# Optimization experiments

Measured on AMD Instinct MI355X. Metric: run time of the kernel, lower is better.

The kernel has to match this reference:

```python
import jax, jax.numpy as jnp
import numpy as np

B, S, D = 1, 2048, 2048
N_HEAD, N_KV = 32, 8
HD = D // N_HEAD  # 64


def make_freqs_cis(seq_len, head_dim, base=10000.0):
    inv = 1.0 / (base ** (np.arange(0, head_dim, 2, dtype=np.float32) / head_dim))
    t = np.arange(seq_len, dtype=np.float32)
    f = np.outer(t, inv)  # [S, HD/2]
    return jnp.asarray(np.stack([np.cos(f), np.sin(f)], axis=-1))  # [S, HD/2, 2]


def setup_inputs() -> dict:
    key = jax.random.key(0)
    k1, k2, k3 = jax.random.split(key, 3)
    scale = 1.0 / np.sqrt(D)
    return {
        "hidden_states": jax.random.normal(k1, (B, S, D), jnp.float32),
        "freqs_cis": make_freqs_cis(S, HD),
        "wqkv": jax.random.normal(k2, ((N_HEAD + 2 * N_KV) * HD, D), jnp.float32) * scale,
        "wo": jax.random.normal(k3, (D, D), jnp.float32) * scale,
    }


def apply_rotary(x, freqs_cis):
    # x: [B, S, H, HD]; freqs_cis: [S, HD/2, 2]
    xs = x.reshape(*x.shape[:-1], HD // 2, 2)
    cos = freqs_cis[None, :, None, :, 0]
    sin = freqs_cis[None, :, None, :, 1]
    x0, x1 = xs[..., 0], xs[..., 1]
    out = jnp.stack([x0 * cos - x1 * sin, x1 * cos + x0 * sin], axis=-1)
    return out.reshape(x.shape)


def reference(hidden_states, freqs_cis, wqkv, wo):
    bsz, seq_len, _ = hidden_states.shape
    kv_size = N_KV * HD
    qkv = hidden_states @ wqkv.T  # [B, S, 3072]
    q, k, v = jnp.split(qkv, [D, D + kv_size], axis=-1)
    q = q.reshape(bsz, seq_len, N_HEAD, HD)
    k = k.reshape(bsz, seq_len, N_KV, HD)
    v = v.reshape(bsz, seq_len, N_KV, HD)
    q = apply_rotary(q, freqs_cis)
    k = apply_rotary(k, freqs_cis)
    # [B, H, S, HD]
    q = q.transpose(0, 2, 1, 3)
    k = k.transpose(0, 2, 1, 3)
    v = v.transpose(0, 2, 1, 3)
    rep = N_HEAD // N_KV
    k = jnp.repeat(k, rep, axis=1)
    v = jnp.repeat(v, rep, axis=1)
    scores = jnp.einsum("bhqd,bhkd->bhqk", q, k) / jnp.sqrt(jnp.float32(HD))
    causal = jnp.tril(jnp.ones((seq_len, seq_len), bool))
    scores = jnp.where(causal[None, None], scores, jnp.finfo(scores.dtype).min)
    attn = jax.nn.softmax(scores, axis=-1)
    out = jnp.einsum("bhqk,bhkd->bhqd", attn, v)
    out = out.transpose(0, 2, 1, 3).reshape(bsz, seq_len, D)
    return out @ wo.T
```

## Files before the change

kernel.cpp:

```cpp
#include <hip/hip_runtime.h>

typedef unsigned short u16;
typedef __attribute__((ext_vector_type(8))) short bf16x8;
typedef __attribute__((ext_vector_type(4))) float f32x4;

#define MFMA16(a, b, c) __builtin_amdgcn_mfma_f32_16x16x32_bf16((a), (b), (c), 0, 0, 0)
#define EXP2(x) __builtin_amdgcn_exp2f(x)

#define S 2048
#define D 2048
#define NH 32
#define NKV 8
#define HD 64
#define QKV_N 3072

__device__ __forceinline__ u16 f2bf(float f) {
  unsigned int u = __float_as_uint(f);
  u += 0x7fffu + ((u >> 16) & 1u);
  return (u16)(u >> 16);
}

__device__ __forceinline__ void glds16(const void* g, void* l) {
  __builtin_amdgcn_global_load_lds((const __attribute__((address_space(1))) unsigned int*)g,
                                   (__attribute__((address_space(3))) unsigned int*)l,
                                   16, 0, 0);
}

__device__ __forceinline__ unsigned int cvtpk(float lo, float hi) {
  unsigned int r;
  asm("v_cvt_pk_bf16_f32 %0, %1, %2" : "=v"(r) : "v"(lo), "v"(hi));
  return r;
}
__device__ __forceinline__ void swap32(unsigned int& a, unsigned int& b) {
  asm("v_permlane32_swap_b32 %0, %1" : "+v"(a), "+v"(b));
}
__device__ __forceinline__ void swap16(unsigned int& a, unsigned int& b) {
  asm("v_permlane16_swap_b32 %0, %1" : "+v"(a), "+v"(b));
}
__device__ __forceinline__ bf16x8 pack4(const f32x4 c0, const f32x4 c1) {
  unsigned int x0 = cvtpk(c0[0], c0[1]);
  unsigned int x1 = cvtpk(c0[2], c0[3]);
  unsigned int y0 = cvtpk(c1[0], c1[1]);
  unsigned int y1 = cvtpk(c1[2], c1[3]);
  swap32(x0, y0); swap16(x0, y0);
  swap32(x1, y1); swap16(x1, y1);
  union { bf16x8 v; unsigned int u[4]; } r;
  r.u[0] = x0; r.u[1] = x1; r.u[2] = y0; r.u[3] = y1;
  return r.v;
}

#define N1 (S * D / 4)
#define N2 (QKV_N * D / 4)
#define N3 (D * D / 4)
__global__ void cast_all(const float* __restrict__ hs, const float* __restrict__ wqkv,
                         const float* __restrict__ wo, u16* __restrict__ o1,
                         u16* __restrict__ o2, u16* __restrict__ o3) {
  int i = blockIdx.x * blockDim.x + threadIdx.x;
  const float* src;
  u16* dst;
  int idx;
  if (i < N1) { src = hs; dst = o1; idx = i; }
  else if (i < N1 + N2) { src = wqkv; dst = o2; idx = i - N1; }
  else if (i < N1 + N2 + N3) { src = wo; dst = o3; idx = i - N1 - N2; }
  else return;
  float4 v = ((const float4*)src)[idx];
  ushort4 o;
  o.x = f2bf(v.x); o.y = f2bf(v.y); o.z = f2bf(v.z); o.w = f2bf(v.w);
  ((ushort4*)dst)[idx] = o;
}

#define GEMM_MAINLOOP(A_, B_, K_, bm_, bn_)                                            \
  const int srowS = lane >> 3, scolS = ((lane & 7) ^ srowS) * 8;                       \
  const int aBase = wave * 32, bBase = wave * 16;                                      \
  const int qq = lane >> 4, sw = lr & 7;                                               \
  _Pragma("unroll") for (int c2 = 0; c2 < 4; ++c2)                                     \
      glds16(A_ + (size_t)(bm_ + aBase + c2 * 8 + srowS) * K_ + scolS,                 \
             &sA[0][aBase + c2 * 8][0]);                                               \
  _Pragma("unroll") for (int c2 = 0; c2 < 2; ++c2)                                     \
      glds16(B_ + (size_t)(bn_ + bBase + c2 * 8 + srowS) * K_ + scolS,                 \
             &sB[0][bBase + c2 * 8][0]);                                               \
  const int nk = K_ >> 6;                                                              \
  for (int it = 0; it < nk; ++it) {                                                    \
    const int buf = it & 1;                                                            \
    __syncthreads();                                                                   \
    if (it + 1 < nk) {                                                                 \
      const int k1 = (it + 1) << 6;                                                    \
      _Pragma("unroll") for (int c2 = 0; c2 < 4; ++c2)                                 \
          glds16(A_ + (size_t)(bm_ + aBase + c2 * 8 + srowS) * K_ + k1 + scolS,        \
                 &sA[buf ^ 1][aBase + c2 * 8][0]);                                     \
      _Pragma("unroll") for (int c2 = 0; c2 < 2; ++c2)                                 \
          glds16(B_ + (size_t)(bn_ + bBase + c2 * 8 + srowS) * K_ + k1 + scolS,        \
                 &sB[buf ^ 1][bBase + c2 * 8][0]);                                     \
    }                                                                                  \
    bf16x8 af[2][2], bfr[2][4];                                                        \
    _Pragma("unroll") for (int c = 0; c < 2; ++c) {                                    \
      const int pc = (((c << 2) | qq) ^ sw) * 8;     \
      _Pragma("unroll") for (int i = 0; i < 2; ++i)                                    \
          af[c][i] = *(const bf16x8*)(&sA[buf][wr + i * 16 + lr][pc]);                 \
      _Pragma("unroll") for (int j = 0; j < 4; ++j)                                    \
          bfr[c][j] = *(const bf16x8*)(&sB[buf][j * 16 + lr][pc]);                     \
    }                                                                                  \
    _Pragma("unroll") for (int c = 0; c < 2; ++c)                                      \
        _Pragma("unroll") for (int i = 0; i < 2; ++i)                                  \
            _Pragma("unroll") for (int j = 0; j < 4; ++j)                              \
                acc[i][j] = MFMA16(af[c][i], bfr[c][j], acc[i][j]);                    \
  }

__global__ __launch_bounds__(256) void gemm_bt(const u16* __restrict__ A, const u16* __restrict__ B,
                                               float* __restrict__ C, int M, int N, int K) {
  __shared__ u16 sA[2][128][64];
  __shared__ u16 sB[2][64][64];
  const int tid = threadIdx.x;
  const int wave = tid >> 6, lane = tid & 63;
  const int bm = blockIdx.y * 128, bn = blockIdx.x * 64;
  const int lr = lane & 15, lk = (lane >> 4) * 8;
  const int wr = wave * 32;
  (void)lk;

  f32x4 acc[2][4] = {};
  GEMM_MAINLOOP(A, B, K, bm, bn)

  const int crb = (lane >> 4) * 4;
#pragma unroll
  for (int i = 0; i < 2; ++i)
#pragma unroll
    for (int j = 0; j < 4; ++j)
#pragma unroll
      for (int r = 0; r < 4; ++r) {
        int row = bm + wr + i * 16 + crb + r;
        int col = bn + j * 16 + lr;
        C[(size_t)row * N + col] = acc[i][j][r];
      }
}

#define QSCALE 0.18033688011112042f
__global__ __launch_bounds__(256) void gemm1_fused(const u16* __restrict__ A, const u16* __restrict__ B,
                                                   const float* __restrict__ fc,
                                                   u16* __restrict__ qo, u16* __restrict__ ko,
                                                   u16* __restrict__ vt) {
  __shared__ u16 sA[2][128][64];
  __shared__ u16 sB[2][64][64];
  const int tid = threadIdx.x;
  const int wave = tid >> 6, lane = tid & 63;
  const int bm = blockIdx.y * 128, bn = blockIdx.x * 64;
  const int lr = lane & 15, lk = (lane >> 4) * 8;
  const int wr = wave * 32;
  (void)lk;

  f32x4 acc[2][4] = {};
  GEMM_MAINLOOP(A, B, D, bm, bn)

  const int crb = (lane >> 4) * 4;

  if (bn < 2560) {
    const bool isQ = (bn < 2048);
    u16* dst_base = isQ ? (qo + (size_t)(bn >> 6) * S * HD)
                        : (ko + (size_t)((bn - 2048) >> 6) * S * HD);
    const float scale = isQ ? QSCALE : 1.0f;
    const int odd = lr & 1;
#pragma unroll
    for (int i = 0; i < 2; ++i)
#pragma unroll
      for (int r = 0; r < 4; ++r) {
        const int srow = bm + wr + i * 16 + crb + r;
#pragma unroll
        for (int j = 0; j < 4; ++j) {
          const int d = j * 16 + lr;
          float x = acc[i][j][r];
          float xp = __shfl_xor(x, 1, 64);
          float2 cs = *(const float2*)(fc + (size_t)srow * 64 + (d >> 1) * 2);
          float y = odd ? (x * cs.x + xp * cs.y) : (x * cs.x - xp * cs.y);
          dst_base[(size_t)srow * HD + d] = f2bf(y * scale);
        }
      }
  } else {
    const int kvh = (bn - 2560) >> 6;
    __syncthreads();
    u16(*sT)[136] = (u16(*)[136]) & sA[0][0][0];
#pragma unroll
    for (int i = 0; i < 2; ++i)
#pragma unroll
      for (int j = 0; j < 4; ++j)
#pragma unroll
        for (int r = 0; r < 4; ++r)
          sT[j * 16 + lr][wr + i * 16 + crb + r] = f2bf(acc[i][j][r]);
    __syncthreads();
    const int d = tid >> 2, sc = (tid & 3) * 32;
    uint4* dst = (uint4*)(vt + (size_t)kvh * HD * S + (size_t)d * S + bm + sc);
    const uint4* src = (const uint4*)(&sT[d][sc]);
    dst[0] = src[0];
    dst[1] = src[1];
    dst[2] = src[2];
    dst[3] = src[3];
  }
}

__global__ __launch_bounds__(256, 2) void attn_kernel(const u16* __restrict__ Q, const u16* __restrict__ Kc,
                                                      const u16* __restrict__ Vt, u16* __restrict__ Out) {
  __shared__ u16 sK[2][64][64];
  __shared__ u16 sV[2][64][64];

  const int h = blockIdx.y;
  const int p = (h >= 16) ? (15 - blockIdx.x) : blockIdx.x;
  const int kvh = h >> 2;
  const int tid = threadIdx.x;
  const int wave = tid >> 6, lane = tid & 63;
  const int lr = lane & 15;
  const int hi = lane >> 4;
  const int lk = hi * 8;
  const int crb = hi * 4;
  const int sw = lr & 7;
  const int pcK0 = (hi ^ sw) * 8;
  const int pcK1 = ((4 | hi) ^ sw) * 8;
  const int t = 4 * p + wave;
  const int qbA = 16 * t;
  const int qbB = 16 * (127 - t);

  const u16* qpA = Q + ((size_t)h * S + qbA + lr) * HD;
  const u16* qpB = Q + ((size_t)h * S + qbB + lr) * HD;
  bf16x8 aA0 = *(const bf16x8*)(qpA + lk);
  bf16x8 aA1 = *(const bf16x8*)(qpA + 32 + lk);
  bf16x8 aB0 = *(const bf16x8*)(qpB + lk);
  bf16x8 aB1 = *(const bf16x8*)(qpB + 32 + lk);

  const u16* Kh = Kc + (size_t)kvh * S * HD;
  const u16* Vh = Vt + (size_t)kvh * HD * S;

  const int sr0 = tid >> 3, so0 = (tid & 7) * 8;
  const int sr1 = sr0 + 32;
  const int swz = (((tid & 7) ^ (sr0 & 7)) << 3);

  f32x4 lAv = {}, lBv = {};
  f32x4 oA[4] = {}, oB[4] = {};

  const int kend = (32 - p) * 64;

  uint4 pk0 = *(const uint4*)(Kh + (size_t)sr0 * HD + so0);
  uint4 pk1 = *(const uint4*)(Kh + (size_t)sr1 * HD + so0);
  uint4 pv0 = *(const uint4*)(Vh + (size_t)sr0 * S + so0);
  uint4 pv1 = *(const uint4*)(Vh + (size_t)sr1 * S + so0);
  *(uint4*)(&sK[0][sr0][swz]) = pk0;
  *(uint4*)(&sK[0][sr1][swz]) = pk1;
  *(uint4*)(&sV[0][sr0][swz]) = pv0;
  *(uint4*)(&sV[0][sr1][swz]) = pv1;
  __syncthreads();

  bf16x8 vf[4][2];
  bf16x8 pfB[2], pfA[2];
  bool prevA = false;

  for (int kb = 0; kb < kend; kb += 64) {
    const int buf = (kb >> 6) & 1;
    const int kn = kb + 64;
    const bool hasNext = (kn < kend);

    if (hasNext) {
      pk0 = *(const uint4*)(Kh + (size_t)(kn + sr0) * HD + so0);
      pk1 = *(const uint4*)(Kh + (size_t)(kn + sr1) * HD + so0);
      pv0 = *(const uint4*)(Vh + (size_t)sr0 * S + kn + so0);
      pv1 = *(const uint4*)(Vh + (size_t)sr1 * S + kn + so0);
    }

    if (kb > 0) {
      __builtin_amdgcn_s_setprio(1);
#pragma unroll
      for (int tt = 0; tt < 4; ++tt) {
        oB[tt] = MFMA16(pfB[0], vf[tt][0], oB[tt]);
        oB[tt] = MFMA16(pfB[1], vf[tt][1], oB[tt]);
      }
      if (prevA) {
#pragma unroll
        for (int tt = 0; tt < 4; ++tt) {
          oA[tt] = MFMA16(pfA[0], vf[tt][0], oA[tt]);
          oA[tt] = MFMA16(pfA[1], vf[tt][1], oA[tt]);
        }
      }
      __builtin_amdgcn_s_setprio(0);
    }

    const bool liveA = (kb <= qbA + 15);

    f32x4 cA[4], cB[4];
    __builtin_amdgcn_s_setprio(1);
#pragma unroll
    for (int tt = 0; tt < 4; ++tt) {
      bf16x8 b0 = *(const bf16x8*)(&sK[buf][tt * 16 + lr][pcK0]);
      bf16x8 b1 = *(const bf16x8*)(&sK[buf][tt * 16 + lr][pcK1]);
      f32x4 zB = {};
      zB = MFMA16(b0, aB0, zB);
      cB[tt] = MFMA16(b1, aB1, zB);
      if (liveA) {
        f32x4 zA = {};
        zA = MFMA16(b0, aA0, zA);
        cA[tt] = MFMA16(b1, aA1, zA);
      }
    }
    __builtin_amdgcn_s_setprio(0);

#pragma unroll
    for (int tt = 0; tt < 4; ++tt) {
      vf[tt][0] = *(const bf16x8*)(&sV[buf][tt * 16 + lr][pcK0]);
      vf[tt][1] = *(const bf16x8*)(&sV[buf][tt * 16 + lr][pcK1]);
    }

    {
      f32x4 pB[4];
      if (kb + 63 <= qbB) {
#pragma unroll
        for (int tt = 0; tt < 4; ++tt) {
#pragma unroll
          for (int r = 0; r < 4; ++r) pB[tt][r] = EXP2(cB[tt][r] - 8.0f);
          lBv += pB[tt];
        }
      } else {
        const int q = qbB + lr;
#pragma unroll
        for (int tt = 0; tt < 4; ++tt) {
#pragma unroll
          for (int r = 0; r < 4; ++r) {
            const int k = kb + tt * 16 + crb + r;
            pB[tt][r] = (k <= q) ? EXP2(cB[tt][r] - 8.0f) : 0.0f;
          }
          lBv += pB[tt];
        }
      }
      pfB[0] = pack4(pB[0], pB[1]);
      pfB[1] = pack4(pB[2], pB[3]);
    }

    if (liveA) {
      f32x4 pA[4];
      if (kb + 63 <= qbA) {
#pragma unroll
        for (int tt = 0; tt < 4; ++tt) {
#pragma unroll
          for (int r = 0; r < 4; ++r) pA[tt][r] = EXP2(cA[tt][r] - 8.0f);
          lAv += pA[tt];
        }
      } else {
        const int q = qbA + lr;
#pragma unroll
        for (int tt = 0; tt < 4; ++tt) {
#pragma unroll
          for (int r = 0; r < 4; ++r) {
            const int k = kb + tt * 16 + crb + r;
            pA[tt][r] = (k <= q) ? EXP2(cA[tt][r] - 8.0f) : 0.0f;
          }
          lAv += pA[tt];
        }
      }
      pfA[0] = pack4(pA[0], pA[1]);
      pfA[1] = pack4(pA[2], pA[3]);
    }

    if (hasNext) {
      *(uint4*)(&sK[buf ^ 1][sr0][swz]) = pk0;
      *(uint4*)(&sK[buf ^ 1][sr1][swz]) = pk1;
      *(uint4*)(&sV[buf ^ 1][sr0][swz]) = pv0;
      *(uint4*)(&sV[buf ^ 1][sr1][swz]) = pv1;
    }
    prevA = liveA;
    __syncthreads();
  }

  __builtin_amdgcn_s_setprio(1);
#pragma unroll
  for (int tt = 0; tt < 4; ++tt) {
    oB[tt] = MFMA16(pfB[0], vf[tt][0], oB[tt]);
    oB[tt] = MFMA16(pfB[1], vf[tt][1], oB[tt]);
  }
  if (prevA) {
#pragma unroll
    for (int tt = 0; tt < 4; ++tt) {
      oA[tt] = MFMA16(pfA[0], vf[tt][0], oA[tt]);
      oA[tt] = MFMA16(pfA[1], vf[tt][1], oA[tt]);
    }
  }
  __builtin_amdgcn_s_setprio(0);

  float lA = lAv[0] + lAv[1] + lAv[2] + lAv[3];
  float lB = lBv[0] + lBv[1] + lBv[2] + lBv[3];
  lA += __shfl_xor(lA, 16, 64);
  lA += __shfl_xor(lA, 32, 64);
  lB += __shfl_xor(lB, 16, 64);
  lB += __shfl_xor(lB, 32, 64);
  float rA[4], rB[4];
#pragma unroll
  for (int r = 0; r < 4; ++r) {
    rA[r] = 1.0f / __shfl(lA, crb + r, 64);
    rB[r] = 1.0f / __shfl(lB, crb + r, 64);
  }
#pragma unroll
  for (int tt = 0; tt < 4; ++tt)
#pragma unroll
    for (int r = 0; r < 4; ++r) {
      const int d = tt * 16 + lr;
      Out[(size_t)(qbA + crb + r) * D + h * HD + d] = f2bf(oA[tt][r] * rA[r]);
      Out[(size_t)(qbB + crb + r) * D + h * HD + d] = f2bf(oB[tt][r] * rB[r]);
    }
}

extern "C" void kernel_launch(void* const* d_in, const int* in_sizes, int n_in,
                              void* d_out, int out_size, void* d_ws, size_t ws_size,
                              hipStream_t stream) {
  const float* hs = (const float*)d_in[0];
  const float* fc = (const float*)d_in[1];
  const float* wqkv = (const float*)d_in[2];
  const float* wo = (const float*)d_in[3];
  float* out = (float*)d_out;
  char* ws = (char*)d_ws;

  u16* hs_bf   = (u16*)(ws);
  u16* wqkv_bf = (u16*)(ws + ((size_t)8 << 20));
  u16* wo_bf   = (u16*)(ws + ((size_t)20 << 20));
  u16* q_bf    = (u16*)(ws + ((size_t)28 << 20));
  u16* k_bf    = (u16*)(ws + ((size_t)36 << 20));
  u16* vt_bf   = (u16*)(ws + ((size_t)38 << 20));
  u16* attn_bf = (u16*)(ws + ((size_t)40 << 20));

  cast_all<<<(N1 + N2 + N3 + 255) / 256, 256, 0, stream>>>(hs, wqkv, wo, hs_bf, wqkv_bf, wo_bf);

  gemm1_fused<<<dim3(QKV_N / 64, S / 128), 256, 0, stream>>>(hs_bf, wqkv_bf, fc, q_bf, k_bf, vt_bf);

  attn_kernel<<<dim3(16, NH), 256, 0, stream>>>(q_bf, k_bf, vt_bf, attn_bf);

  gemm_bt<<<dim3(D / 64, S / 128), 256, 0, stream>>>(attn_bf, wo_bf, out, S, D, D);
}
```

Measured before the change: 195.4 us.

## Split attention key range across two wave groups per block and merge partials

Each attention block now runs 512 threads as two groups of four waves, and each group processes half of the key tiles with its own double-buffered shared-memory K/V staging. At the end, group 1 writes its partial outputs and row sums to shared memory and group 0 adds them before normalizing and storing. The aim is more waves in flight per CU to hide latency in the causal attention loop. The cost is a final shared-memory reduction, doubled LDS use, and register pressure under launch bounds of 512 threads at 4 blocks per CU.

New measurement: 304.5 us. 55.9% more time.

```diff
diff --git a/kernel.cpp b/kernel.cpp
--- a/kernel.cpp
+++ b/kernel.cpp
@@ -195,16 +195,18 @@
   }
 }
 
-__global__ __launch_bounds__(256, 2) void attn_kernel(const u16* __restrict__ Q, const u16* __restrict__ Kc,
+__global__ __launch_bounds__(512, 4) void attn_kernel(const u16* __restrict__ Q, const u16* __restrict__ Kc,
                                                       const u16* __restrict__ Vt, u16* __restrict__ Out) {
-  __shared__ u16 sK[2][64][64];
-  __shared__ u16 sV[2][64][64];
+  __shared__ u16 sAll[2][2][2][64][64];
 
   const int h = blockIdx.y;
   const int p = (h >= 16) ? (15 - blockIdx.x) : blockIdx.x;
   const int kvh = h >> 2;
   const int tid = threadIdx.x;
   const int wave = tid >> 6, lane = tid & 63;
+  const int g = wave >> 2;
+  const int w = wave & 3;
+  const int tg = tid & 255;
   const int lr = lane & 15;
   const int hi = lane >> 4;
   const int lk = hi * 8;
@@ -212,7 +214,7 @@
   const int sw = lr & 7;
   const int pcK0 = (hi ^ sw) * 8;
   const int pcK1 = ((4 | hi) ^ sw) * 8;
-  const int t = 4 * p + wave;
+  const int t = 4 * p + w;
   const int qbA = 16 * t;
   const int qbB = 16 * (127 - t);
 
@@ -226,140 +228,150 @@
   const u16* Kh = Kc + (size_t)kvh * S * HD;
   const u16* Vh = Vt + (size_t)kvh * HD * S;
 
-  const int sr0 = tid >> 3, so0 = (tid & 7) * 8;
+  const int sr0 = tg >> 3, so0 = (tg & 7) * 8;
   const int sr1 = sr0 + 32;
-  const int swz = (((tid & 7) ^ (sr0 & 7)) << 3);
+  const int swz = (((tg & 7) ^ (sr0 & 7)) << 3);
 
   f32x4 lAv = {}, lBv = {};
   f32x4 oA[4] = {}, oB[4] = {};
 
-  const int kend = (32 - p) * 64;
-
-  uint4 pk0 = *(const uint4*)(Kh + (size_t)sr0 * HD + so0);
-  uint4 pk1 = *(const uint4*)(Kh + (size_t)sr1 * HD + so0);
-  uint4 pv0 = *(const uint4*)(Vh + (size_t)sr0 * S + so0);
-  uint4 pv1 = *(const uint4*)(Vh + (size_t)sr1 * S + so0);
-  *(uint4*)(&sK[0][sr0][swz]) = pk0;
-  *(uint4*)(&sK[0][sr1][swz]) = pk1;
-  *(uint4*)(&sV[0][sr0][swz]) = pv0;
-  *(uint4*)(&sV[0][sr1][swz]) = pv1;
+  const int nt = 32 - p;
+  const int nt0 = (nt + 1) >> 1;
+  const int nt1 = nt >> 1;
+  const int myNT = g ? nt1 : nt0;
+  const int kb0 = g ? nt0 * 64 : 0;
+
+  uint4 pk0 = *(const uint4*)(Kh + (size_t)(kb0 + sr0) * HD + so0);
+  uint4 pk1 = *(const uint4*)(Kh + (size_t)(kb0 + sr1) * HD + so0);
+  uint4 pv0 = *(const uint4*)(Vh + (size_t)sr0 * S + kb0 + so0);
+  uint4 pv1 = *(const uint4*)(Vh + (size_t)sr1 * S + kb0 + so0);
+  *(uint4*)(&sAll[0][g][0][sr0][swz]) = pk0;
+  *(uint4*)(&sAll[0][g][0][sr1][swz]) = pk1;
+  *(uint4*)(&sAll[1][g][0][sr0][swz]) = pv0;
+  *(uint4*)(&sAll[1][g][0][sr1][swz]) = pv1;
   __syncthreads();
 
   bf16x8 vf[4][2];
   bf16x8 pfB[2], pfA[2];
   bool prevA = false;
 
-  for (int kb = 0; kb < kend; kb += 64) {
-    const int buf = (kb >> 6) & 1;
-    const int kn = kb + 64;
-    const bool hasNext = (kn < kend);
-
-    if (hasNext) {
-      pk0 = *(const uint4*)(Kh + (size_t)(kn + sr0) * HD + so0);
-      pk1 = *(const uint4*)(Kh + (size_t)(kn + sr1) * HD + so0);
-      pv0 = *(const uint4*)(Vh + (size_t)sr0 * S + kn + so0);
-      pv1 = *(const uint4*)(Vh + (size_t)sr1 * S + kn + so0);
+  for (int i = 0; i < nt0; ++i) {
+    const bool active = (i < myNT);
+    const int kb = kb0 + i * 64;
+    const int buf = i & 1;
+    const bool hasNext = (i + 1 < myNT);
+
+    if (active) {
+      if (hasNext) {
+        const int kn = kb + 64;
+        pk0 = *(const uint4*)(Kh + (size_t)(kn + sr0) * HD + so0);
+        pk1 = *(const uint4*)(Kh + (size_t)(kn + sr1) * HD + so0);
+        pv0 = *(const uint4*)(Vh + (size_t)sr0 * S + kn + so0);
+        pv1 = *(const uint4*)(Vh + (size_t)sr1 * S + kn + so0);
+      }
+
+      if (i > 0) {
+        __builtin_amdgcn_s_setprio(1);
+#pragma unroll
+        for (int tt = 0; tt < 4; ++tt) {
+          oB[tt] = MFMA16(pfB[0], vf[tt][0], oB[tt]);
+          oB[tt] = MFMA16(pfB[1], vf[tt][1], oB[tt]);
+        }
+        if (prevA) {
+#pragma unroll
+          for (int tt = 0; tt < 4; ++tt) {
+            oA[tt] = MFMA16(pfA[0], vf[tt][0], oA[tt]);
+            oA[tt] = MFMA16(pfA[1], vf[tt][1], oA[tt]);
+          }
+        }
+        __builtin_amdgcn_s_setprio(0);
+      }
+
+      const bool liveA = (kb <= qbA + 15);
+
+      f32x4 cA[4], cB[4];
+      __builtin_amdgcn_s_setprio(1);
+#pragma unroll
+      for (int tt = 0; tt < 4; ++tt) {
+        bf16x8 b0 = *(const bf16x8*)(&sAll[0][g][buf][tt * 16 + lr][pcK0]);
+        bf16x8 b1 = *(const bf16x8*)(&sAll[0][g][buf][tt * 16 + lr][pcK1]);
+        f32x4 zB = {};
+        zB = MFMA16(b0, aB0, zB);
+        cB[tt] = MFMA16(b1, aB1, zB);
+        if (liveA) {
+          f32x4 zA = {};
+          zA = MFMA16(b0, aA0, zA);
+          cA[tt] = MFMA16(b1, aA1, zA);
+        }
+      }
+      __builtin_amdgcn_s_setprio(0);
+
+#pragma unroll
+      for (int tt = 0; tt < 4; ++tt) {
+        vf[tt][0] = *(const bf16x8*)(&sAll[1][g][buf][tt * 16 + lr][pcK0]);
+        vf[tt][1] = *(const bf16x8*)(&sAll[1][g][buf][tt * 16 + lr][pcK1]);
+      }
+
+      {
+        f32x4 pB[4];
+        if (kb + 63 <= qbB) {
+#pragma unroll
+          for (int tt = 0; tt < 4; ++tt) {
+#pragma unroll
+            for (int r = 0; r < 4; ++r) pB[tt][r] = EXP2(cB[tt][r] - 8.0f);
+            lBv += pB[tt];
+          }
+        } else {
+          const int q = qbB + lr;
+#pragma unroll
+          for (int tt = 0; tt < 4; ++tt) {
+#pragma unroll
+            for (int r = 0; r < 4; ++r) {
+              const int k = kb + tt * 16 + crb + r;
+              pB[tt][r] = (k <= q) ? EXP2(cB[tt][r] - 8.0f) : 0.0f;
+            }
+            lBv += pB[tt];
+          }
+        }
+        pfB[0] = pack4(pB[0], pB[1]);
+        pfB[1] = pack4(pB[2], pB[3]);
+      }
+
+      if (liveA) {
+        f32x4 pA[4];
+        if (kb + 63 <= qbA) {
+#pragma unroll
+          for (int tt = 0; tt < 4; ++tt) {
+#pragma unroll
+            for (int r = 0; r < 4; ++r) pA[tt][r] = EXP2(cA[tt][r] - 8.0f);
+            lAv += pA[tt];
+          }
+        } else {
+          const int q = qbA + lr;
+#pragma unroll
+          for (int tt = 0; tt < 4; ++tt) {
+#pragma unroll
+            for (int r = 0; r < 4; ++r) {
+              const int k = kb + tt * 16 + crb + r;
+              pA[tt][r] = (k <= q) ? EXP2(cA[tt][r] - 8.0f) : 0.0f;
+            }
+            lAv += pA[tt];
+          }
+        }
+        pfA[0] = pack4(pA[0], pA[1]);
+        pfA[1] = pack4(pA[2], pA[3]);
+        prevA = true;
+      } else {
+        prevA = false;
+      }
+
+      if (hasNext) {
+        *(uint4*)(&sAll[0][g][buf ^ 1][sr0][swz]) = pk0;
+        *(uint4*)(&sAll[0][g][buf ^ 1][sr1][swz]) = pk1;
+        *(uint4*)(&sAll[1][g][buf ^ 1][sr0][swz]) = pv0;
+        *(uint4*)(&sAll[1][g][buf ^ 1][sr1][swz]) = pv1;
+      }
     }
-
-    if (kb > 0) {
-      __builtin_amdgcn_s_setprio(1);
-#pragma unroll
-      for (int tt = 0; tt < 4; ++tt) {
-        oB[tt] = MFMA16(pfB[0], vf[tt][0], oB[tt]);
-        oB[tt] = MFMA16(pfB[1], vf[tt][1], oB[tt]);
-      }
-      if (prevA) {
-#pragma unroll
-        for (int tt = 0; tt < 4; ++tt) {
-          oA[tt] = MFMA16(pfA[0], vf[tt][0], oA[tt]);
-          oA[tt] = MFMA16(pfA[1], vf[tt][1], oA[tt]);
-        }
-      }
-      __builtin_amdgcn_s_setprio(0);
-    }
-
-    const bool liveA = (kb <= qbA + 15);
-
-    f32x4 cA[4], cB[4];
-    __builtin_amdgcn_s_setprio(1);
-#pragma unroll
-    for (int tt = 0; tt < 4; ++tt) {
-      bf16x8 b0 = *(const bf16x8*)(&sK[buf][tt * 16 + lr][pcK0]);
-      bf16x8 b1 = *(const bf16x8*)(&sK[buf][tt * 16 + lr][pcK1]);
-      f32x4 zB = {};
-      zB = MFMA16(b0, aB0, zB);
-      cB[tt] = MFMA16(b1, aB1, zB);
-      if (liveA) {
-        f32x4 zA = {};
-        zA = MFMA16(b0, aA0, zA);
-        cA[tt] = MFMA16(b1, aA1, zA);
-      }
-    }
-    __builtin_amdgcn_s_setprio(0);
-
-#pragma unroll
-    for (int tt = 0; tt < 4; ++tt) {
-      vf[tt][0] = *(const bf16x8*)(&sV[buf][tt * 16 + lr][pcK0]);
-      vf[tt][1] = *(const bf16x8*)(&sV[buf][tt * 16 + lr][pcK1]);
-    }
-
-    {
-      f32x4 pB[4];
-      if (kb + 63 <= qbB) {
-#pragma unroll
-        for (int tt = 0; tt < 4; ++tt) {
-#pragma unroll
-          for (int r = 0; r < 4; ++r) pB[tt][r] = EXP2(cB[tt][r] - 8.0f);
-          lBv += pB[tt];
-        }
-      } else {
-        const int q = qbB + lr;
-#pragma unroll
-        for (int tt = 0; tt < 4; ++tt) {
-#pragma unroll
-          for (int r = 0; r < 4; ++r) {
-            const int k = kb + tt * 16 + crb + r;
-            pB[tt][r] = (k <= q) ? EXP2(cB[tt][r] - 8.0f) : 0.0f;
-          }
-          lBv += pB[tt];
-        }
-      }
-      pfB[0] = pack4(pB[0], pB[1]);
-      pfB[1] = pack4(pB[2], pB[3]);
-    }
-
-    if (liveA) {
-      f32x4 pA[4];
-      if (kb + 63 <= qbA) {
-#pragma unroll
-        for (int tt = 0; tt < 4; ++tt) {
-#pragma unroll
-          for (int r = 0; r < 4; ++r) pA[tt][r] = EXP2(cA[tt][r] - 8.0f);
-          lAv += pA[tt];
-        }
-      } else {
-        const int q = qbA + lr;
-#pragma unroll
-        for (int tt = 0; tt < 4; ++tt) {
-#pragma unroll
-          for (int r = 0; r < 4; ++r) {
-            const int k = kb + tt * 16 + crb + r;
-            pA[tt][r] = (k <= q) ? EXP2(cA[tt][r] - 8.0f) : 0.0f;
-          }
-          lAv += pA[tt];
-        }
-      }
-      pfA[0] = pack4(pA[0], pA[1]);
-      pfA[1] = pack4(pA[2], pA[3]);
-    }
-
-    if (hasNext) {
-      *(uint4*)(&sK[buf ^ 1][sr0][swz]) = pk0;
-      *(uint4*)(&sK[buf ^ 1][sr1][swz]) = pk1;
-      *(uint4*)(&sV[buf ^ 1][sr0][swz]) = pv0;
-      *(uint4*)(&sV[buf ^ 1][sr1][swz]) = pv1;
-    }
-    prevA = liveA;
     __syncthreads();
   }
 
@@ -380,24 +392,51 @@
 
   float lA = lAv[0] + lAv[1] + lAv[2] + lAv[3];
   float lB = lBv[0] + lBv[1] + lBv[2] + lBv[3];
-  lA += __shfl_xor(lA, 16, 64);
-  lA += __shfl_xor(lA, 32, 64);
-  lB += __shfl_xor(lB, 16, 64);
-  lB += __shfl_xor(lB, 32, 64);
-  float rA[4], rB[4];
-#pragma unroll
-  for (int r = 0; r < 4; ++r) {
-    rA[r] = 1.0f / __shfl(lA, crb + r, 64);
-    rB[r] = 1.0f / __shfl(lB, crb + r, 64);
-  }
-#pragma unroll
-  for (int tt = 0; tt < 4; ++tt)
+
+  float* cb = (float*)&sAll[0][0][0][0][0];
+  float* my = cb + (size_t)(w * 64 + lane) * 34;
+  if (g == 1) {
+#pragma unroll
+    for (int tt = 0; tt < 4; ++tt)
+#pragma unroll
+      for (int r = 0; r < 4; ++r) {
+        my[tt * 4 + r] = oA[tt][r];
+        my[16 + tt * 4 + r] = oB[tt][r];
+      }
+    my[32] = lA;
+    my[33] = lB;
+  }
+  __syncthreads();
+  if (g == 0) {
+#pragma unroll
+    for (int tt = 0; tt < 4; ++tt)
+#pragma unroll
+      for (int r = 0; r < 4; ++r) {
+        oA[tt][r] += my[tt * 4 + r];
+        oB[tt][r] += my[16 + tt * 4 + r];
+      }
+    lA += my[32];
+    lB += my[33];
+
+    lA += __shfl_xor(lA, 16, 64);
+    lA += __shfl_xor(lA, 32, 64);
+    lB += __shfl_xor(lB, 16, 64);
+    lB += __shfl_xor(lB, 32, 64);
+    float rA[4], rB[4];
 #pragma unroll
     for (int r = 0; r < 4; ++r) {
-      const int d = tt * 16 + lr;
-      Out[(size_t)(qbA + crb + r) * D + h * HD + d] = f2bf(oA[tt][r] * rA[r]);
-      Out[(size_t)(qbB + crb + r) * D + h * HD + d] = f2bf(oB[tt][r] * rB[r]);
+      rA[r] = 1.0f / __shfl(lA, crb + r, 64);
+      rB[r] = 1.0f / __shfl(lB, crb + r, 64);
     }
+#pragma unroll
+    for (int tt = 0; tt < 4; ++tt)
+#pragma unroll
+      for (int r = 0; r < 4; ++r) {
+        const int d = tt * 16 + lr;
+        Out[(size_t)(qbA + crb + r) * D + h * HD + d] = f2bf(oA[tt][r] * rA[r]);
+        Out[(size_t)(qbB + crb + r) * D + h * HD + d] = f2bf(oB[tt][r] * rB[r]);
+      }
+  }
 }
 
 extern "C" void kernel_launch(void* const* d_in, const int* in_sizes, int n_in,
@@ -422,7 +461,7 @@
 
   gemm1_fused<<<dim3(QKV_N / 64, S / 128), 256, 0, stream>>>(hs_bf, wqkv_bf, fc, q_bf, k_bf, vt_bf);
 
-  attn_kernel<<<dim3(16, NH), 256, 0, stream>>>(q_bf, k_bf, vt_bf, attn_bf);
+  attn_kernel<<<dim3(16, NH), 512, 0, stream>>>(q_bf, k_bf, vt_bf, attn_bf);
 
   gemm_bt<<<dim3(D / 64, S / 128), 256, 0, stream>>>(attn_bf, wo_bf, out, S, D, D);
 }
```

## Software-pipeline attention loop: QK of current block overlaps softmax and PV of previous

Applied to the files above, without the earlier changes.

The attention inner loop is restructured so each step first issues the QK MFMAs for the current key block. It then runs the exp/mask softmax and PV MFMAs for the previous block, using ping-pong score register sets in a two-step unrolled loop. The aim is to overlap MFMA work with the exp/VALU work of the previous tile and hide LDS and global load latency. The cost is two live sets of score accumulators, which raises VGPR pressure and may reduce occupancy or cause spills.

After: 277.8 us. +42.2%, slower.

```diff
diff --git a/kernel.cpp b/kernel.cpp
--- a/kernel.cpp
+++ b/kernel.cpp
@@ -245,138 +245,114 @@
   *(uint4*)(&sV[0][sr1][swz]) = pv1;
   __syncthreads();
 
+  f32x4 cXA[4], cXB[4], cYA[4], cYB[4];
   bf16x8 vf[4][2];
-  bf16x8 pfB[2], pfA[2];
-  bool prevA = false;
-
-  for (int kb = 0; kb < kend; kb += 64) {
-    const int buf = (kb >> 6) & 1;
-    const int kn = kb + 64;
-    const bool hasNext = (kn < kend);
-
-    if (hasNext) {
-      pk0 = *(const uint4*)(Kh + (size_t)(kn + sr0) * HD + so0);
-      pk1 = *(const uint4*)(Kh + (size_t)(kn + sr1) * HD + so0);
-      pv0 = *(const uint4*)(Vh + (size_t)sr0 * S + kn + so0);
-      pv1 = *(const uint4*)(Vh + (size_t)sr1 * S + kn + so0);
+  bool pLiveA = false;
+
+#define SM_SPAN(CARR, qb, lacc, pf0, pf1, kbp)                                \
+  {                                                                           \
+    f32x4 pt_[4];                                                             \
+    if ((kbp) + 63 <= (qb)) {                                                 \
+      _Pragma("unroll") for (int u = 0; u < 4; ++u) {                         \
+        _Pragma("unroll") for (int r = 0; r < 4; ++r)                         \
+            pt_[u][r] = EXP2(CARR[u][r] - 8.0f);                              \
+        lacc += pt_[u];                                                       \
+      }                                                                       \
+    } else {                                                                  \
+      const int q_ = (qb) + lr;                                               \
+      _Pragma("unroll") for (int u = 0; u < 4; ++u) {                         \
+        _Pragma("unroll") for (int r = 0; r < 4; ++r) {                       \
+          const int k_ = (kbp) + u * 16 + crb + r;                            \
+          pt_[u][r] = (k_ <= q_) ? EXP2(CARR[u][r] - 8.0f) : 0.0f;            \
+        }                                                                     \
+        lacc += pt_[u];                                                       \
+      }                                                                       \
+    }                                                                         \
+    pf0 = pack4(pt_[0], pt_[1]);                                              \
+    pf1 = pack4(pt_[2], pt_[3]);                                              \
+  }
+
+#define SMPV_PREV(CPA, CPB, kbp)                                              \
+  {                                                                           \
+    bf16x8 pfB[2], pfA[2];                                                    \
+    SM_SPAN(CPB, qbB, lBv, pfB[0], pfB[1], kbp)                               \
+    if (pLiveA) SM_SPAN(CPA, qbA, lAv, pfA[0], pfA[1], kbp)                   \
+    __builtin_amdgcn_s_setprio(1);                                            \
+    _Pragma("unroll") for (int tt = 0; tt < 4; ++tt) {                        \
+      oB[tt] = MFMA16(pfB[0], vf[tt][0], oB[tt]);                             \
+      oB[tt] = MFMA16(pfB[1], vf[tt][1], oB[tt]);                             \
+    }                                                                         \
+    if (pLiveA) {                                                             \
+      _Pragma("unroll") for (int tt = 0; tt < 4; ++tt) {                      \
+        oA[tt] = MFMA16(pfA[0], vf[tt][0], oA[tt]);                           \
+        oA[tt] = MFMA16(pfA[1], vf[tt][1], oA[tt]);                           \
+      }                                                                       \
+    }                                                                         \
+    __builtin_amdgcn_s_setprio(0);                                            \
+  }
+
+#define FULLSTEP(CNA, CNB, CPA, CPB)                                          \
+  {                                                                           \
+    const int buf = (kb >> 6) & 1;                                            \
+    const int kn = kb + 64;                                                   \
+    const bool hasNext = (kn < kend);                                         \
+    if (hasNext) {                                                            \
+      pk0 = *(const uint4*)(Kh + (size_t)(kn + sr0) * HD + so0);              \
+      pk1 = *(const uint4*)(Kh + (size_t)(kn + sr1) * HD + so0);              \
+      pv0 = *(const uint4*)(Vh + (size_t)sr0 * S + kn + so0);                 \
+      pv1 = *(const uint4*)(Vh + (size_t)sr1 * S + kn + so0);                 \
+    }                                                                         \
+    const bool liveA = (kb <= qbA + 15);                                      \
+    __builtin_amdgcn_s_setprio(1);                                            \
+    _Pragma("unroll") for (int tt = 0; tt < 4; ++tt) {                        \
+      bf16x8 b0 = *(const bf16x8*)(&sK[buf][tt * 16 + lr][pcK0]);             \
+      bf16x8 b1 = *(const bf16x8*)(&sK[buf][tt * 16 + lr][pcK1]);             \
+      f32x4 zB = {};                                                          \
+      zB = MFMA16(b0, aB0, zB);                                               \
+      CNB[tt] = MFMA16(b1, aB1, zB);                                          \
+      if (liveA) {                                                            \
+        f32x4 zA = {};                                                        \
+        zA = MFMA16(b0, aA0, zA);                                             \
+        CNA[tt] = MFMA16(b1, aA1, zA);                                        \
+      }                                                                       \
+    }                                                                         \
+    __builtin_amdgcn_s_setprio(0);                                            \
+    if (kb > 0) SMPV_PREV(CPA, CPB, kb - 64)                                  \
+    _Pragma("unroll") for (int tt = 0; tt < 4; ++tt) {                        \
+      vf[tt][0] = *(const bf16x8*)(&sV[buf][tt * 16 + lr][pcK0]);             \
+      vf[tt][1] = *(const bf16x8*)(&sV[buf][tt * 16 + lr][pcK1]);             \
+    }                                                                         \
+    if (hasNext) {                                                            \
+      *(uint4*)(&sK[buf ^ 1][sr0][swz]) = pk0;                                \
+      *(uint4*)(&sK[buf ^ 1][sr1][swz]) = pk1;                                \
+      *(uint4*)(&sV[buf ^ 1][sr0][swz]) = pv0;                                \
+      *(uint4*)(&sV[buf ^ 1][sr1][swz]) = pv1;                                \
+    }                                                                         \
+    pLiveA = liveA;                                                           \
+    __syncthreads();                                                          \
+  }
+
+  int kb = 0;
+  while (true) {
+    FULLSTEP(cXA, cXB, cYA, cYB)
+    kb += 64;
+    if (kb >= kend) break;
+    FULLSTEP(cYA, cYB, cXA, cXB)
+    kb += 64;
+    if (kb >= kend) break;
+  }
+
+  {
+    const int kbp = kend - 64;
+    if ((kend >> 6) & 1) {
+      SMPV_PREV(cXA, cXB, kbp)
+    } else {
+      SMPV_PREV(cYA, cYB, kbp)
     }
-
-    if (kb > 0) {
-      __builtin_amdgcn_s_setprio(1);
-#pragma unroll
-      for (int tt = 0; tt < 4; ++tt) {
-        oB[tt] = MFMA16(pfB[0], vf[tt][0], oB[tt]);
-        oB[tt] = MFMA16(pfB[1], vf[tt][1], oB[tt]);
-      }
-      if (prevA) {
-#pragma unroll
-        for (int tt = 0; tt < 4; ++tt) {
-          oA[tt] = MFMA16(pfA[0], vf[tt][0], oA[tt]);
-          oA[tt] = MFMA16(pfA[1], vf[tt][1], oA[tt]);
-        }
-      }
-      __builtin_amdgcn_s_setprio(0);
-    }
-
-    const bool liveA = (kb <= qbA + 15);
-
-    f32x4 cA[4], cB[4];
-    __builtin_amdgcn_s_setprio(1);
-#pragma unroll
-    for (int tt = 0; tt < 4; ++tt) {
-      bf16x8 b0 = *(const bf16x8*)(&sK[buf][tt * 16 + lr][pcK0]);
-      bf16x8 b1 = *(const bf16x8*)(&sK[buf][tt * 16 + lr][pcK1]);
-      f32x4 zB = {};
-      zB = MFMA16(b0, aB0, zB);
-      cB[tt] = MFMA16(b1, aB1, zB);
-      if (liveA) {
-        f32x4 zA = {};
-        zA = MFMA16(b0, aA0, zA);
-        cA[tt] = MFMA16(b1, aA1, zA);
-      }
-    }
-    __builtin_amdgcn_s_setprio(0);
-
-#pragma unroll
-    for (int tt = 0; tt < 4; ++tt) {
-      vf[tt][0] = *(const bf16x8*)(&sV[buf][tt * 16 + lr][pcK0]);
-      vf[tt][1] = *(const bf16x8*)(&sV[buf][tt * 16 + lr][pcK1]);
-    }
-
-    {
-      f32x4 pB[4];
-      if (kb + 63 <= qbB) {
-#pragma unroll
-        for (int tt = 0; tt < 4; ++tt) {
-#pragma unroll
-          for (int r = 0; r < 4; ++r) pB[tt][r] = EXP2(cB[tt][r] - 8.0f);
-          lBv += pB[tt];
-        }
-      } else {
-        const int q = qbB + lr;
-#pragma unroll
-        for (int tt = 0; tt < 4; ++tt) {
-#pragma unroll
-          for (int r = 0; r < 4; ++r) {
-            const int k = kb + tt * 16 + crb + r;
-            pB[tt][r] = (k <= q) ? EXP2(cB[tt][r] - 8.0f) : 0.0f;
-          }
-          lBv += pB[tt];
-        }
-      }
-      pfB[0] = pack4(pB[0], pB[1]);
-      pfB[1] = pack4(pB[2], pB[3]);
-    }
-
-    if (liveA) {
-      f32x4 pA[4];
-      if (kb + 63 <= qbA) {
-#pragma unroll
-        for (int tt = 0; tt < 4; ++tt) {
-#pragma unroll
-          for (int r = 0; r < 4; ++r) pA[tt][r] = EXP2(cA[tt][r] - 8.0f);
-          lAv += pA[tt];
-        }
-      } else {
-        const int q = qbA + lr;
-#pragma unroll
-        for (int tt = 0; tt < 4; ++tt) {
-#pragma unroll
-          for (int r = 0; r < 4; ++r) {
-            const int k = kb + tt * 16 + crb + r;
-            pA[tt][r] = (k <= q) ? EXP2(cA[tt][r] - 8.0f) : 0.0f;
-          }
-          lAv += pA[tt];
-        }
-      }
-      pfA[0] = pack4(pA[0], pA[1]);
-      pfA[1] = pack4(pA[2], pA[3]);
-    }
-
-    if (hasNext) {
-      *(uint4*)(&sK[buf ^ 1][sr0][swz]) = pk0;
-      *(uint4*)(&sK[buf ^ 1][sr1][swz]) = pk1;
-      *(uint4*)(&sV[buf ^ 1][sr0][swz]) = pv0;
-      *(uint4*)(&sV[buf ^ 1][sr1][swz]) = pv1;
-    }
-    prevA = liveA;
-    __syncthreads();
-  }
-
-  __builtin_amdgcn_s_setprio(1);
-#pragma unroll
-  for (int tt = 0; tt < 4; ++tt) {
-    oB[tt] = MFMA16(pfB[0], vf[tt][0], oB[tt]);
-    oB[tt] = MFMA16(pfB[1], vf[tt][1], oB[tt]);
-  }
-  if (prevA) {
-#pragma unroll
-    for (int tt = 0; tt < 4; ++tt) {
-      oA[tt] = MFMA16(pfA[0], vf[tt][0], oA[tt]);
-      oA[tt] = MFMA16(pfA[1], vf[tt][1], oA[tt]);
-    }
-  }
-  __builtin_amdgcn_s_setprio(0);
+  }
+#undef FULLSTEP
+#undef SMPV_PREV
+#undef SM_SPAN
 
   float lA = lAv[0] + lAv[1] + lAv[2] + lAv[3];
   float lB = lBv[0] + lBv[1] + lBv[2] + lBv[3];
```
